# Kernel tuning notes

Hardware: AMD Instinct MI355X
Metric: run time of the kernel (lower is better)

## Reference

```python
import jax, jax.numpy as jnp
import numpy as np
import math

PI = math.pi
PATCH_SIZE = 32
NUM_BINS = 36
EPS = 1e-8


def setup_inputs() -> dict:
    key = jax.random.key(0)
    patch = jax.random.normal(key, (65536, 1, PATCH_SIZE, PATCH_SIZE), dtype=jnp.float32)
    return {"patch": patch}


def reference(patch):
    B = patch.shape[0]
    dt = patch.dtype
    # kornia SpatialGradient('sobel', 1): L1-normalized sobel kernels, replicate padding
    kx = jnp.array([[-1.0, 0.0, 1.0], [-2.0, 0.0, 2.0], [-1.0, 0.0, 1.0]], dtype=dt) / 8.0
    ky = kx.T
    kernel = jnp.stack([kx, ky])[:, None]  # [2,1,3,3] OIHW
    padded = jnp.pad(patch, ((0, 0), (0, 0), (1, 1), (1, 1)), mode="edge")
    grads = jax.lax.conv_general_dilated(
        padded, kernel, window_strides=(1, 1), padding="VALID",
        dimension_numbers=("NCHW", "OIHW", "NCHW"))  # [B,2,H,W]
    gx, gy = grads[:, 0], grads[:, 1]
    mag = jnp.sqrt(gx * gx + gy * gy + EPS)
    ori = jnp.arctan2(gy, gx + EPS) + 2.0 * PI
    o_big = float(NUM_BINS) * (ori + PI) / (2.0 * PI)
    bo0 = jnp.floor(o_big)
    wo1 = o_big - bo0
    b0 = (bo0 % NUM_BINS).astype(jnp.int32)
    b1 = (b0 + 1) % NUM_BINS
    w0 = (1.0 - wo1) * mag
    w1 = wo1 * mag
    npix = PATCH_SIZE * PATCH_SIZE
    # soft histogram via scatter-add; adaptive_avg_pool2d(1,1) == mean over pixels
    def histo(b0f, b1f, w0f, w1f):
        return jnp.zeros(NUM_BINS, dtype=dt).at[b0f].add(w0f).at[b1f].add(w1f)
    hist = jax.vmap(histo)(b0.reshape(B, -1), b1.reshape(B, -1),
                           w0.reshape(B, -1), w1.reshape(B, -1)) / npix
    # circular conv1d with fixed kernel [0.33, 0.34, 0.33]
    sm = 0.33 * jnp.roll(hist, 1, axis=-1) + 0.34 * hist + 0.33 * jnp.roll(hist, -1, axis=-1)
    indices = jnp.argmax(sm, axis=-1)
    angle = -(2.0 * PI * indices.astype(dt) / float(NUM_BINS) - PI)
    return angle
```

## Files before the change

kernel.cpp:

```cpp
#include <hip/hip_runtime.h>
#include <math.h>

#pragma clang fp contract(off)

#define NBINS 36
#define PS 32

__device__ __forceinline__ float atan2_np(float fy, float fx)
{
    const double aT0  =  3.33333333333329318027e-01;
    const double aT1  = -1.99999999998764832476e-01;
    const double aT2  =  1.42857142725034663711e-01;
    const double aT3  = -1.11111104054623557880e-01;
    const double aT4  =  9.09088713343650656196e-02;
    const double aT5  = -7.69187620504482999495e-02;
    const double aT6  =  6.66107313738753120669e-02;
    const double aT7  = -5.83357013379057348645e-02;
    const double aT8  =  4.97687799461593236017e-02;
    const double aT9  = -3.65315727442169155270e-02;
    const double aT10 =  1.62858201153657823623e-02;

    double y = (double)fy, x = (double)fx;
    double ax = fabs(x), ay = fabs(y);
    double u = fmax(ax, ay);
    double v = fmin(ax, ay);

    bool g1 = v >= 0.4375 * u;
    bool g2 = v >= 0.6875 * u;
    double c      = g2 ? 1.0 : (g1 ? 0.5 : 0.0);
    double atc_hi = g2 ? 7.85398163397448278999e-01
                       : (g1 ? 4.63647609000806093515e-01 : 0.0);
    double atc_lo = g2 ? 3.06161699786838301793e-17
                       : (g1 ? 2.26987774529616870924e-17 : 0.0);

    double num = fma(-c, u, v);
    double den = fma(c, v, u);

    double r0 = __builtin_amdgcn_rcp(den);
    r0 = fma(fma(-den, r0, 1.0), r0, r0);
    r0 = fma(fma(-den, r0, 1.0), r0, r0);
    double q0 = num * r0;
    double xq = fma(fma(-den, q0, num), r0, q0);

    double z = xq * xq;
    double w = z * z;
    double s1 = z * fma(w, fma(w, fma(w, fma(w, fma(w, aT10, aT8), aT6), aT4), aT2), aT0);
    double s2 = w * fma(w, fma(w, fma(w, fma(w, aT9, aT7), aT5), aT3), aT1);
    double p  = xq * (s1 + s2);
    double res = atc_hi - ((p - atc_lo) - xq);

    double res2 = (1.57079632679489655800e+00 - res) + 6.12323399573676603587e-17;
    res = (ay > ax) ? res2 : res;
    double res3 = (3.14159265358979311600e+00 - res) + 1.22464679914735317723e-16;
    res = (x < 0.0) ? res3 : res;
    res = copysign(res, y);
    return (float)res;
}

__global__ __launch_bounds__(256)
void patch_orient_kernel(const float* __restrict__ patches, float* __restrict__ out)
{
    __shared__ __align__(16) float tile[PS][PS];
    __shared__ unsigned bm[PS][NBINS];
    __shared__ unsigned short pref[PS][NBINS];
    __shared__ unsigned short cnt[NBINS];
    __shared__ unsigned short start[NBINS];
    __shared__ __align__(16) float s0[1024];
    __shared__ __align__(16) float s1[1024];
    __shared__ float hsm[NBINS];

    const int t = threadIdx.x;
    const int b = blockIdx.x;
    const float* p = patches + (size_t)b * (PS * PS);

    #pragma unroll
    for (int i = t; i < PS * NBINS; i += 256) ((unsigned*)bm)[i] = 0u;

    ((float4*)tile)[t] = ((const float4*)p)[t];
    __syncthreads();

    const int row = t >> 3;
    const int cb  = (t & 7) << 2;
    const int rm  = (row == 0)  ? 0  : row - 1;
    const int rp  = (row == 31) ? 31 : row + 1;

    float win[3][6];
    {
        const int cl = (cb == 0)  ? 0  : cb - 1;
        const int cr = (cb == 28) ? 31 : cb + 4;
        const int rows[3] = {rm, row, rp};
        #pragma unroll
        for (int r = 0; r < 3; ++r) {
            float4 v = *((const float4*)&tile[rows[r]][cb]);
            win[r][0] = tile[rows[r]][cl];
            win[r][1] = v.x; win[r][2] = v.y; win[r][3] = v.z; win[r][4] = v.w;
            win[r][5] = tile[rows[r]][cr];
        }
    }

    const float TWO_PI = 6.2831853071795864769f;
    const float PI_F   = 3.14159265358979323846f;

    float w0r[4], w1r[4];
    int   binr[4];

    #pragma unroll
    for (int i = 0; i < 4; ++i) {
        float A = win[0][i], B = win[0][i + 1], C = win[0][i + 2];
        float D = win[1][i],                    F = win[1][i + 2];
        float G = win[2][i], H = win[2][i + 1], I = win[2][i + 2];

        float gx = -0.125f * A;
        gx += 0.125f  * C;
        gx += -0.25f  * D;
        gx += 0.25f   * F;
        gx += -0.125f * G;
        gx += 0.125f  * I;

        float gy = -0.125f * A;
        gy += -0.25f  * B;
        gy += -0.125f * C;
        gy += 0.125f  * G;
        gy += 0.25f   * H;
        gy += 0.125f  * I;

        float m1 = gx * gx;
        float m2 = gy * gy;
        float s  = m1 + m2;
        s = s + 1e-8f;
        float mag = sqrtf(s);

        float gxe = gx + 1e-8f;
        float at  = atan2_np(gy, gxe);
        float ori = at + TWO_PI;
        float obig = (36.0f * (ori + PI_F)) / TWO_PI;
        float bo0  = floorf(obig);
        float wo1  = obig - bo0;

        int bi0 = (int)bo0 - 36;
        if (bi0 < 0)   bi0 += 36;
        if (bi0 >= 36) bi0 -= 36;

        w0r[i]  = (1.0f - wo1) * mag;
        w1r[i]  = wo1 * mag;
        binr[i] = bi0;
        atomicOr(&bm[row][bi0], 1u << (cb + i));
    }
    __syncthreads();

    if (t < 64) {
        unsigned run = 0;
        if (t < NBINS) {
            #pragma unroll 1
            for (int w = 0; w < PS; ++w) {
                pref[w][t] = (unsigned short)run;
                run += __popc(bm[w][t]);
            }
            cnt[t] = (unsigned short)run;
        }
        unsigned v = run;
        #pragma unroll
        for (int d = 1; d < 64; d <<= 1) {
            unsigned o = (unsigned)__shfl_up((int)v, d);
            if (t >= d) v += o;
        }
        if (t < NBINS) start[t] = (unsigned short)(v - run);
    }
    __syncthreads();

    #pragma unroll
    for (int i = 0; i < 4; ++i) {
        const int bi = binr[i];
        const unsigned lowmask = (1u << (cb + i)) - 1u;
        const int pos = (int)start[bi] + (int)pref[row][bi]
                      + __popc(bm[row][bi] & lowmask);
        s0[pos] = w0r[i];
        s1[pos] = w1r[i];
    }
    __syncthreads();

    if (t < NBINS) {
        float acc = 0.0f;
        {
            int st = start[t], en = st + cnt[t];
            int i = st;
            for (; i + 1 < en; i += 2) { acc += s0[i]; acc += s0[i + 1]; }
            if (i < en) acc += s0[i];
        }
        {
            int t2 = (t == 0) ? NBINS - 1 : t - 1;
            int st = start[t2], en = st + cnt[t2];
            int i = st;
            for (; i + 1 < en; i += 2) { acc += s1[i]; acc += s1[i + 1]; }
            if (i < en) acc += s1[i];
        }
        hsm[t] = acc * (1.0f / 1024.0f);
    }
    __syncthreads();

    if (t == 0) {
        float best = -1.0f; int bi = 0;
        #pragma unroll
        for (int i = 0; i < NBINS; ++i) {
            int im_ = (i == 0)         ? NBINS - 1 : i - 1;
            int ip_ = (i == NBINS - 1) ? 0         : i + 1;
            float q0 = 0.33f * hsm[im_];
            float q1 = 0.34f * hsm[i];
            float q2 = 0.33f * hsm[ip_];
            float sm = (q0 + q1) + q2;
            if (sm > best) { best = sm; bi = i; }
        }
        float t1 = TWO_PI * (float)bi;
        float t2 = t1 / 36.0f;
        float t3 = t2 - PI_F;
        out[b] = -t3;
    }
}

extern "C" void kernel_launch(void* const* d_in, const int* in_sizes, int n_in,
                              void* d_out, int out_size, void* d_ws, size_t ws_size,
                              hipStream_t stream) {
    const float* patch = (const float*)d_in[0];
    float* out = (float*)d_out;
    const int B = in_sizes[0] / (PS * PS);
    patch_orient_kernel<<<B, 256, 0, stream>>>(patch, out);
}
```

Measured before the change: 532.5 us.

## Simplify atan2 reduction, transpose bin bitmap, vectorize prefix and reductions, wave-parallel argmax

The atan2 range reduction now uses a single threshold at tan(pi/8) computed in float, dropping the three-way split and some double conversions. The bin bitmap is transposed to bin-major with padding so each bin's row words can be read as uint4, and row prefix counts are packed two per 32-bit word. Histogram accumulation uses aligned float4 reads from shared memory, and the serial argmax over 36 bins on one thread becomes a wave shuffle reduction with lowest-index tie-breaking. Together these aim to cut serial shared-memory latency and double-precision ALU work, though the changed reduction interval may shift atan2 rounding slightly.

Result: slower. 550.1 us (+3.3%).

```diff
diff --git a/kernel.cpp b/kernel.cpp
--- a/kernel.cpp
+++ b/kernel.cpp
@@ -20,18 +20,14 @@
     const double aT9  = -3.65315727442169155270e-02;
     const double aT10 =  1.62858201153657823623e-02;
 
-    double y = (double)fy, x = (double)fx;
-    double ax = fabs(x), ay = fabs(y);
-    double u = fmax(ax, ay);
-    double v = fmin(ax, ay);
-
-    bool g1 = v >= 0.4375 * u;
-    bool g2 = v >= 0.6875 * u;
-    double c      = g2 ? 1.0 : (g1 ? 0.5 : 0.0);
-    double atc_hi = g2 ? 7.85398163397448278999e-01
-                       : (g1 ? 4.63647609000806093515e-01 : 0.0);
-    double atc_lo = g2 ? 3.06161699786838301793e-17
-                       : (g1 ? 2.26987774529616870924e-17 : 0.0);
+    float axf = fabsf(fx), ayf = fabsf(fy);
+    float uf = fmaxf(axf, ayf), vf = fminf(axf, ayf);
+    bool g1 = vf >= 0.41421356f * uf;
+
+    double u = (double)uf, v = (double)vf;
+    double c      = g1 ? 1.0 : 0.0;
+    double atc_hi = g1 ? 7.85398163397448278999e-01 : 0.0;
+    double atc_lo = g1 ? 3.06161699786838301793e-17 : 0.0;
 
     double num = fma(-c, u, v);
     double den = fma(c, v, u);
@@ -44,16 +40,16 @@
 
     double z = xq * xq;
     double w = z * z;
-    double s1 = z * fma(w, fma(w, fma(w, fma(w, fma(w, aT10, aT8), aT6), aT4), aT2), aT0);
-    double s2 = w * fma(w, fma(w, fma(w, fma(w, aT9, aT7), aT5), aT3), aT1);
-    double p  = xq * (s1 + s2);
+    double s1_ = z * fma(w, fma(w, fma(w, fma(w, fma(w, aT10, aT8), aT6), aT4), aT2), aT0);
+    double s2_ = w * fma(w, fma(w, fma(w, fma(w, aT9, aT7), aT5), aT3), aT1);
+    double p   = xq * (s1_ + s2_);
     double res = atc_hi - ((p - atc_lo) - xq);
 
     double res2 = (1.57079632679489655800e+00 - res) + 6.12323399573676603587e-17;
-    res = (ay > ax) ? res2 : res;
+    res = (ayf > axf) ? res2 : res;
     double res3 = (3.14159265358979311600e+00 - res) + 1.22464679914735317723e-16;
-    res = (x < 0.0) ? res3 : res;
-    res = copysign(res, y);
+    res = (fx < 0.0f) ? res3 : res;
+    res = copysign(res, (double)fy);
     return (float)res;
 }
 
@@ -61,8 +57,8 @@
 void patch_orient_kernel(const float* __restrict__ patches, float* __restrict__ out)
 {
     __shared__ __align__(16) float tile[PS][PS];
-    __shared__ unsigned bm[PS][NBINS];
-    __shared__ unsigned short pref[PS][NBINS];
+    __shared__ __align__(16) unsigned bm[NBINS][36];
+    __shared__ __align__(16) unsigned pref32[NBINS][16];
     __shared__ unsigned short cnt[NBINS];
     __shared__ unsigned short start[NBINS];
     __shared__ __align__(16) float s0[1024];
@@ -74,7 +70,7 @@
     const float* p = patches + (size_t)b * (PS * PS);
 
     #pragma unroll
-    for (int i = t; i < PS * NBINS; i += 256) ((unsigned*)bm)[i] = 0u;
+    for (int i = t; i < NBINS * 32; i += 256) bm[i >> 5][i & 31] = 0u;
 
     ((float4*)tile)[t] = ((const float4*)p)[t];
     __syncthreads();
@@ -144,17 +140,33 @@
         w0r[i]  = (1.0f - wo1) * mag;
         w1r[i]  = wo1 * mag;
         binr[i] = bi0;
-        atomicOr(&bm[row][bi0], 1u << (cb + i));
+        atomicOr(&bm[bi0][row], 1u << (cb + i));
     }
     __syncthreads();
 
     if (t < 64) {
         unsigned run = 0;
         if (t < NBINS) {
-            #pragma unroll 1
-            for (int w = 0; w < PS; ++w) {
-                pref[w][t] = (unsigned short)run;
-                run += __popc(bm[w][t]);
+            const uint4* bw = (const uint4*)&bm[t][0];
+            uint4* pw = (uint4*)&pref32[t][0];
+            #pragma unroll
+            for (int k = 0; k < 4; ++k) {
+                uint4 wa = bw[2 * k], wb = bw[2 * k + 1];
+                unsigned p0 = run;
+                unsigned p1 = p0 + __popc(wa.x);
+                unsigned p2 = p1 + __popc(wa.y);
+                unsigned p3 = p2 + __popc(wa.z);
+                unsigned p4 = p3 + __popc(wa.w);
+                unsigned p5 = p4 + __popc(wb.x);
+                unsigned p6 = p5 + __popc(wb.y);
+                unsigned p7 = p6 + __popc(wb.z);
+                run = p7 + __popc(wb.w);
+                uint4 pk;
+                pk.x = p0 | (p1 << 16);
+                pk.y = p2 | (p3 << 16);
+                pk.z = p4 | (p5 << 16);
+                pk.w = p6 | (p7 << 16);
+                pw[k] = pk;
             }
             cnt[t] = (unsigned short)run;
         }
@@ -171,9 +183,11 @@
     #pragma unroll
     for (int i = 0; i < 4; ++i) {
         const int bi = binr[i];
+        unsigned pv = pref32[bi][row >> 1];
+        pv = (row & 1) ? (pv >> 16) : (pv & 0xffffu);
         const unsigned lowmask = (1u << (cb + i)) - 1u;
-        const int pos = (int)start[bi] + (int)pref[row][bi]
-                      + __popc(bm[row][bi] & lowmask);
+        const int pos = (int)start[bi] + (int)pv
+                      + __popc(bm[bi][row] & lowmask);
         s0[pos] = w0r[i];
         s1[pos] = w1r[i];
     }
@@ -182,38 +196,53 @@
     if (t < NBINS) {
         float acc = 0.0f;
         {
-            int st = start[t], en = st + cnt[t];
-            int i = st;
-            for (; i + 1 < en; i += 2) { acc += s0[i]; acc += s0[i + 1]; }
-            if (i < en) acc += s0[i];
+            int i = start[t], en = i + cnt[t];
+            int lim = (i + 3) & ~3; if (lim > en) lim = en;
+            for (; i < lim; ++i) acc += s0[i];
+            for (; i + 4 <= en; i += 4) {
+                float4 v4 = *((const float4*)&s0[i]);
+                acc += v4.x; acc += v4.y; acc += v4.z; acc += v4.w;
+            }
+            for (; i < en; ++i) acc += s0[i];
         }
         {
             int t2 = (t == 0) ? NBINS - 1 : t - 1;
-            int st = start[t2], en = st + cnt[t2];
-            int i = st;
-            for (; i + 1 < en; i += 2) { acc += s1[i]; acc += s1[i + 1]; }
-            if (i < en) acc += s1[i];
+            int i = start[t2], en = i + cnt[t2];
+            int lim = (i + 3) & ~3; if (lim > en) lim = en;
+            for (; i < lim; ++i) acc += s1[i];
+            for (; i + 4 <= en; i += 4) {
+                float4 v4 = *((const float4*)&s1[i]);
+                acc += v4.x; acc += v4.y; acc += v4.z; acc += v4.w;
+            }
+            for (; i < en; ++i) acc += s1[i];
         }
         hsm[t] = acc * (1.0f / 1024.0f);
     }
     __syncthreads();
 
-    if (t == 0) {
-        float best = -1.0f; int bi = 0;
+    if (t < 64) {
+        float val = -1.0f;
+        int   idx = t;
+        if (t < NBINS) {
+            int im_ = (t == 0)         ? NBINS - 1 : t - 1;
+            int ip_ = (t == NBINS - 1) ? 0         : t + 1;
+            float q0 = 0.33f * hsm[im_];
+            float q1 = 0.34f * hsm[t];
+            float q2 = 0.33f * hsm[ip_];
+            val = (q0 + q1) + q2;
+        }
         #pragma unroll
-        for (int i = 0; i < NBINS; ++i) {
-            int im_ = (i == 0)         ? NBINS - 1 : i - 1;
-            int ip_ = (i == NBINS - 1) ? 0         : i + 1;
-            float q0 = 0.33f * hsm[im_];
-            float q1 = 0.34f * hsm[i];
-            float q2 = 0.33f * hsm[ip_];
-            float sm = (q0 + q1) + q2;
-            if (sm > best) { best = sm; bi = i; }
-        }
-        float t1 = TWO_PI * (float)bi;
-        float t2 = t1 / 36.0f;
-        float t3 = t2 - PI_F;
-        out[b] = -t3;
+        for (int d = 1; d < 64; d <<= 1) {
+            float ov = __shfl_xor(val, d);
+            int   oi = __shfl_xor(idx, d);
+            if (ov > val || (ov == val && oi < idx)) { val = ov; idx = oi; }
+        }
+        if (t == 0) {
+            float t1 = TWO_PI * (float)idx;
+            float t2 = t1 / 36.0f;
+            float t3 = t2 - PI_F;
+            out[b] = -t3;
+        }
     }
 }
 
```
